# Kernel optimization log

Hardware: AMD Instinct MI355X
Metric: run time of the kernel (lower is better)

The kernel has to match this reference:

```python
import jax, jax.numpy as jnp
import numpy as np

EPS_LN = 1e-10
EPS_NORM = 0.001


def setup_inputs() -> dict:
    key = jax.random.key(0)
    ks = jax.random.split(key, 6)
    B, L, F, P, ZO = 1, 512, 64, 32, 128
    M = jax.random.normal(ks[0], (B, L, F), dtype=jnp.float32)
    M_mask = jnp.ones((B, L), dtype=jnp.float32)
    gamma = jnp.ones((F,), dtype=jnp.float32)
    beta = jnp.zeros((F,), dtype=jnp.float32)
    # glorot-uniform-ish scales
    Wa = jax.random.uniform(ks[1], (P, F), jnp.float32, -0.25, 0.25)
    ba = jnp.zeros((P,), jnp.float32)
    Wb = jax.random.uniform(ks[2], (P, F), jnp.float32, -0.25, 0.25)
    bb = jnp.zeros((P,), jnp.float32)
    # linear_z is zero-init in the original; use small random so output is nontrivial
    Wz = jax.random.uniform(ks[3], (ZO, P * P), jnp.float32, -0.04, 0.04)
    bz = jnp.zeros((ZO,), jnp.float32)
    return {"M": M, "M_mask": M_mask, "gamma": gamma, "beta": beta,
            "Wa": Wa, "ba": ba, "Wb": Wb, "bb": bb, "Wz": Wz, "bz": bz}


def reference(M, M_mask, gamma, beta, Wa, ba, Wb, bb, Wz, bz):
    # LayerNorm over last dim (custom: std = sqrt(var + eps))
    mean = jnp.mean(M, axis=-1, keepdims=True)
    var = jnp.mean((M - mean) ** 2, axis=-1, keepdims=True)
    y = (M - mean) / jnp.sqrt(var + EPS_LN) * gamma + beta  # (B, L, F)
    mask = M_mask[..., None]  # (B, L, 1)
    a = (jnp.einsum('blf,pf->blp', y, Wa) + ba) * mask  # (B, L, P)
    b = (jnp.einsum('blf,pf->blp', y, Wb) + bb) * mask  # (B, L, P)
    B_, L, P = a.shape
    # outer product over pairs (s dim of original einsum is size 1)
    O = jnp.einsum('bid,bje->bijde', a, b).reshape(B_, L, L, P * P)
    Z = jnp.einsum('bijk,zk->bijz', O, Wz) + bz  # (B, L, L, n_feat_out)
    norm = (M_mask[:, :, None] * M_mask[:, None, :])[..., None]  # (B, L, L, 1)
    return Z / (EPS_NORM + norm)
```

## Files before the change

### kernel.cpp

```cpp
#include <hip/hip_runtime.h>
#include <hip/hip_bf16.h>

#define L  512
#define F  64
#define P  32
#define ZO 128
#define JCH 16
#define LZ (L * ZO)

constexpr float EPS_LN   = 1e-10f;
constexpr float EPS_NORM = 1e-3f;

typedef short s16x8 __attribute__((ext_vector_type(8)));
typedef float f32x4 __attribute__((ext_vector_type(4)));

__global__ __launch_bounds__(256) void k_ln_proj(
    const float* __restrict__ M, const float* __restrict__ mask,
    const float* __restrict__ gamma, const float* __restrict__ beta,
    const float* __restrict__ Wa, const float* __restrict__ ba,
    const float* __restrict__ Wb, const float* __restrict__ bb,
    float* __restrict__ a, float* __restrict__ b,
    __hip_bfloat16* __restrict__ abf) {
  __shared__ float y_lds[4][F];
  const int wave = threadIdx.x >> 6;
  const int lane = threadIdx.x & 63;
  const int row  = blockIdx.x * 4 + wave;

  float m = M[row * F + lane];
  float s = m;
  #pragma unroll
  for (int o = 32; o >= 1; o >>= 1) s += __shfl_xor(s, o);
  float mean = s * (1.0f / F);
  float d = m - mean;
  float v = d * d;
  #pragma unroll
  for (int o = 32; o >= 1; o >>= 1) v += __shfl_xor(v, o);
  float rstd = rsqrtf(v * (1.0f / F) + EPS_LN);
  float y = d * rstd * gamma[lane] + beta[lane];
  y_lds[wave][lane] = y;
  __syncthreads();

  const float mk = mask[row];
  const float* W    = (lane < P) ? Wa : Wb;
  const float* bias = (lane < P) ? ba : bb;
  const int p = lane & (P - 1);
  float acc = 0.f;
  #pragma unroll 8
  for (int f = 0; f < F; ++f) acc += y_lds[wave][f] * W[p * F + f];
  acc = (acc + bias[p]) * mk;
  if (lane < P) {
    a[row * P + p]   = acc;
    abf[row * P + p] = __float2bfloat16(acc);
  } else {
    b[row * P + p] = acc;
  }
}

__global__ __launch_bounds__(256) void k_T(
    const float* __restrict__ b, const float* __restrict__ Wz,
    __hip_bfloat16* __restrict__ Tbf) {
  const int seg = blockIdx.x * 256 + threadIdx.x;
  const int j0  = blockIdx.y * JCH;

  float4 w[8];
  const float4* wp = (const float4*)(Wz + (size_t)seg * 32);
  #pragma unroll
  for (int q = 0; q < 8; ++q) w[q] = wp[q];

  #pragma unroll 2
  for (int jj = 0; jj < JCH; ++jj) {
    const float* __restrict__ br = b + (size_t)(j0 + jj) * P;
    float acc0 = 0.f, acc1 = 0.f, acc2 = 0.f, acc3 = 0.f;
    #pragma unroll
    for (int q = 0; q < 8; ++q) {
      acc0 += w[q].x * br[q * 4 + 0];
      acc1 += w[q].y * br[q * 4 + 1];
      acc2 += w[q].z * br[q * 4 + 2];
      acc3 += w[q].w * br[q * 4 + 3];
    }
    Tbf[(size_t)(j0 + jj) * (ZO * P) + seg] =
        __float2bfloat16((acc0 + acc1) + (acc2 + acc3));
  }
}

__global__ __launch_bounds__(256, 8) void k_z(
    const __hip_bfloat16* __restrict__ abf,
    const float* __restrict__ mask,
    const __hip_bfloat16* __restrict__ Tbf,
    const float* __restrict__ bz,
    float* __restrict__ Z) {
  const int t    = threadIdx.x;
  const int lane = t & 63;
  const int w    = t >> 6;
  const int r16  = lane & 15;
  const int kg   = lane >> 4;
  const int bx   = blockIdx.x;
  const int sx   = (bx & 7) * 32 + (bx >> 3);
  const int ngg  = sx & 63;
  const int qc   = sx >> 6;
  const int i0   = blockIdx.y * 16;
  const int ng   = ngg * 4 + w;
  const int n0   = ng * 256;

  const s16x8 afrag =
      *(const s16x8*)((const short*)abf + (size_t)(i0 + r16) * P + kg * 8);

  const int jj = (n0 >> 7) + (qc >> 1);
  const float mj = mask[jj];
  const float4 mi4 = *(const float4*)(mask + i0 + kg * 4);
  float inv[4];
  inv[0] = __builtin_amdgcn_rcpf(EPS_NORM + mi4.x * mj);
  inv[1] = __builtin_amdgcn_rcpf(EPS_NORM + mi4.y * mj);
  inv[2] = __builtin_amdgcn_rcpf(EPS_NORM + mi4.z * mj);
  inv[3] = __builtin_amdgcn_rcpf(EPS_NORM + mi4.w * mj);

  float bzr[4];
  #pragma unroll
  for (int k2 = 0; k2 < 4; ++k2)
    bzr[k2] = bz[(((qc * 4 + k2) & 7) * 16) + r16];

  const short* tb = (const short*)Tbf + (size_t)(n0 + r16) * P + kg * 8;
  float* zb = Z + (size_t)(i0 + kg * 4) * LZ + n0 + r16;

  #pragma unroll
  for (int k2 = 0; k2 < 4; ++k2) {
    const int q = qc * 4 + k2;
    const s16x8 bfrag = *(const s16x8*)(tb + (size_t)q * 16 * P);
    f32x4 acc = {0.f, 0.f, 0.f, 0.f};
    acc = __builtin_amdgcn_mfma_f32_16x16x32_bf16(afrag, bfrag, acc, 0, 0, 0);
    const float bzv = bzr[k2];
    float* zq = zb + q * 16;
    zq[(size_t)0 * LZ] = (acc[0] + bzv) * inv[0];
    zq[(size_t)1 * LZ] = (acc[1] + bzv) * inv[1];
    zq[(size_t)2 * LZ] = (acc[2] + bzv) * inv[2];
    zq[(size_t)3 * LZ] = (acc[3] + bzv) * inv[3];
  }
}

extern "C" void kernel_launch(void* const* d_in, const int* in_sizes, int n_in,
                              void* d_out, int out_size, void* d_ws, size_t ws_size,
                              hipStream_t stream) {
  const float* M     = (const float*)d_in[0];
  const float* mask  = (const float*)d_in[1];
  const float* gamma = (const float*)d_in[2];
  const float* beta  = (const float*)d_in[3];
  const float* Wa    = (const float*)d_in[4];
  const float* ba    = (const float*)d_in[5];
  const float* Wb    = (const float*)d_in[6];
  const float* bb    = (const float*)d_in[7];
  const float* Wz    = (const float*)d_in[8];
  const float* bz    = (const float*)d_in[9];

  float* Z = (float*)d_out;
  float* a = (float*)d_ws;
  float* b = a + L * P;
  __hip_bfloat16* Tbf = (__hip_bfloat16*)(b + L * P);
  __hip_bfloat16* abf = Tbf + (size_t)L * ZO * P;

  k_ln_proj<<<L / 4, 256, 0, stream>>>(M, mask, gamma, beta, Wa, ba, Wb, bb,
                                       a, b, abf);
  k_T<<<dim3((ZO * P) / 256, L / JCH), 256, 0, stream>>>(b, Wz, Tbf);
  k_z<<<dim3(256, 32), 256, 0, stream>>>(abf, mask, Tbf, bz, Z);
}
```

Baseline: 38.93 us.

## Fuse LayerNorm/projection into the T kernel, recomputing b rows per block

Merges the LayerNorm+projection kernel into the Wz-contraction kernel. Each block recomputes LayerNorm and the b projection for its 16 rows into LDS, and blocks with blockIdx.x==0 also produce the bf16 a rows. This removes one kernel launch and the global round trip for b. In exchange the LN/projection work is repeated across the 16 x-blocks, and the a-producing blocks carry extra work, which creates load imbalance.

```diff
diff --git a/kernel.cpp b/kernel.cpp
--- a/kernel.cpp
+++ b/kernel.cpp
@@ -14,54 +14,69 @@
 typedef short s16x8 __attribute__((ext_vector_type(8)));
 typedef float f32x4 __attribute__((ext_vector_type(4)));
 
-__global__ __launch_bounds__(256) void k_ln_proj(
+__global__ __launch_bounds__(256) void k_lnT(
     const float* __restrict__ M, const float* __restrict__ mask,
     const float* __restrict__ gamma, const float* __restrict__ beta,
     const float* __restrict__ Wa, const float* __restrict__ ba,
     const float* __restrict__ Wb, const float* __restrict__ bb,
-    float* __restrict__ a, float* __restrict__ b,
-    __hip_bfloat16* __restrict__ abf) {
-  __shared__ float y_lds[4][F];
-  const int wave = threadIdx.x >> 6;
-  const int lane = threadIdx.x & 63;
-  const int row  = blockIdx.x * 4 + wave;
+    const float* __restrict__ Wz,
+    __hip_bfloat16* __restrict__ Tbf, __hip_bfloat16* __restrict__ abf) {
+  __shared__ float y_sh[4][F];
+  __shared__ float b_lds[JCH][P];
+  const int t    = threadIdx.x;
+  const int wave = t >> 6;
+  const int lane = t & 63;
+  const int j0   = blockIdx.y * JCH;
 
-  float m = M[row * F + lane];
-  float s = m;
   #pragma unroll
-  for (int o = 32; o >= 1; o >>= 1) s += __shfl_xor(s, o);
-  float mean = s * (1.0f / F);
-  float d = m - mean;
-  float v = d * d;
-  #pragma unroll
-  for (int o = 32; o >= 1; o >>= 1) v += __shfl_xor(v, o);
-  float rstd = rsqrtf(v * (1.0f / F) + EPS_LN);
-  float y = d * rstd * gamma[lane] + beta[lane];
-  y_lds[wave][lane] = y;
+  for (int rr = 0; rr < 4; ++rr) {
+    const int row = j0 + wave * 4 + rr;
+    const float m = M[row * F + lane];
+    float s = m;
+    #pragma unroll
+    for (int o = 32; o >= 1; o >>= 1) s += __shfl_xor(s, o);
+    const float mean = s * (1.0f / F);
+    const float d = m - mean;
+    float v = d * d;
+    #pragma unroll
+    for (int o = 32; o >= 1; o >>= 1) v += __shfl_xor(v, o);
+    const float rstd = rsqrtf(v * (1.0f / F) + EPS_LN);
+    y_sh[wave][lane] = d * rstd * gamma[lane] + beta[lane];
+    const int p = lane & (P - 1);
+    float acc = 0.f;
+    #pragma unroll 8
+    for (int f = 0; f < F; ++f) acc += y_sh[wave][f] * Wb[p * F + f];
+    if (lane < P) b_lds[wave * 4 + rr][p] = (acc + bb[p]) * mask[row];
+  }
+
+  if (blockIdx.x == 0) {
+    const int i0 = blockIdx.y * 16;
+    #pragma unroll
+    for (int rr = 0; rr < 4; ++rr) {
+      const int row = i0 + wave * 4 + rr;
+      const float m = M[row * F + lane];
+      float s = m;
+      #pragma unroll
+      for (int o = 32; o >= 1; o >>= 1) s += __shfl_xor(s, o);
+      const float mean = s * (1.0f / F);
+      const float d = m - mean;
+      float v = d * d;
+      #pragma unroll
+      for (int o = 32; o >= 1; o >>= 1) v += __shfl_xor(v, o);
+      const float rstd = rsqrtf(v * (1.0f / F) + EPS_LN);
+      y_sh[wave][lane] = d * rstd * gamma[lane] + beta[lane];
+      const int p = lane & (P - 1);
+      float acc = 0.f;
+      #pragma unroll 8
+      for (int f = 0; f < F; ++f) acc += y_sh[wave][f] * Wa[p * F + f];
+      if (lane < P)
+        abf[row * P + p] = __float2bfloat16((acc + ba[p]) * mask[row]);
+    }
+  }
+
   __syncthreads();
 
-  const float mk = mask[row];
-  const float* W    = (lane < P) ? Wa : Wb;
-  const float* bias = (lane < P) ? ba : bb;
-  const int p = lane & (P - 1);
-  float acc = 0.f;
-  #pragma unroll 8
-  for (int f = 0; f < F; ++f) acc += y_lds[wave][f] * W[p * F + f];
-  acc = (acc + bias[p]) * mk;
-  if (lane < P) {
-    a[row * P + p]   = acc;
-    abf[row * P + p] = __float2bfloat16(acc);
-  } else {
-    b[row * P + p] = acc;
-  }
-}
-
-__global__ __launch_bounds__(256) void k_T(
-    const float* __restrict__ b, const float* __restrict__ Wz,
-    __hip_bfloat16* __restrict__ Tbf) {
-  const int seg = blockIdx.x * 256 + threadIdx.x;
-  const int j0  = blockIdx.y * JCH;
-
+  const int seg = blockIdx.x * 256 + t;
   float4 w[8];
   const float4* wp = (const float4*)(Wz + (size_t)seg * 32);
   #pragma unroll
@@ -69,14 +84,13 @@
 
   #pragma unroll 2
   for (int jj = 0; jj < JCH; ++jj) {
-    const float* __restrict__ br = b + (size_t)(j0 + jj) * P;
     float acc0 = 0.f, acc1 = 0.f, acc2 = 0.f, acc3 = 0.f;
     #pragma unroll
     for (int q = 0; q < 8; ++q) {
-      acc0 += w[q].x * br[q * 4 + 0];
-      acc1 += w[q].y * br[q * 4 + 1];
-      acc2 += w[q].z * br[q * 4 + 2];
-      acc3 += w[q].w * br[q * 4 + 3];
+      acc0 += w[q].x * b_lds[jj][q * 4 + 0];
+      acc1 += w[q].y * b_lds[jj][q * 4 + 1];
+      acc2 += w[q].z * b_lds[jj][q * 4 + 2];
+      acc3 += w[q].w * b_lds[jj][q * 4 + 3];
     }
     Tbf[(size_t)(j0 + jj) * (ZO * P) + seg] =
         __float2bfloat16((acc0 + acc1) + (acc2 + acc3));
@@ -152,13 +166,10 @@
   const float* bz    = (const float*)d_in[9];
 
   float* Z = (float*)d_out;
-  float* a = (float*)d_ws;
-  float* b = a + L * P;
-  __hip_bfloat16* Tbf = (__hip_bfloat16*)(b + L * P);
+  __hip_bfloat16* Tbf = (__hip_bfloat16*)d_ws;
   __hip_bfloat16* abf = Tbf + (size_t)L * ZO * P;
 
-  k_ln_proj<<<L / 4, 256, 0, stream>>>(M, mask, gamma, beta, Wa, ba, Wb, bb,
-                                       a, b, abf);
-  k_T<<<dim3((ZO * P) / 256, L / JCH), 256, 0, stream>>>(b, Wz, Tbf);
+  k_lnT<<<dim3((ZO * P) / 256, L / JCH), 256, 0, stream>>>(
+      M, mask, gamma, beta, Wa, ba, Wb, bb, Wz, Tbf, abf);
   k_z<<<dim3(256, 32), 256, 0, stream>>>(abf, mask, Tbf, bz, Z);
 }
```

Result: slower. 64.80 us (+66.5%).
